# Kernel tuning notes

Measured on AMD Instinct MI355X. Metric: run time of the kernel, lower is better.

## Reference

```python
import jax, jax.numpy as jnp
import numpy as np

RANK = 32
ALPHA = 1.0
SCALE = ALPHA / RANK


def setup_inputs() -> dict:
    key = jax.random.key(0)
    k1, k2, k3, k4, k5 = jax.random.split(key, 5)
    B_, S, D_in, D_out = 4, 2048, 4096, 4096
    x = jax.random.normal(k1, (B_, S, D_in), dtype=jnp.float32)
    # nn.Linear weight: [out, in], kaiming-ish scale
    W = jax.random.normal(k2, (D_out, D_in), dtype=jnp.float32) / np.sqrt(D_in)
    bias = jax.random.normal(k3, (D_out,), dtype=jnp.float32) * 0.01
    A = jax.random.normal(k4, (D_in, RANK), dtype=jnp.float32) * 0.01
    # torch init is zeros for B; use small random so output depends on LoRA path
    Bm = jax.random.normal(k5, (RANK, D_out), dtype=jnp.float32) * 0.01
    return {"x": x, "W": W, "bias": bias, "A": A, "B": Bm}


def reference(x, W, bias, A, B):
    # Original: y = x @ (W + scale*(A@B)^T)^T + bias
    # Mathematically identical fused form (two GEMMs, no [in,out] delta):
    base = jnp.einsum('bsd,od->bso', x, W)          # [B,S,out]
    lora = jnp.einsum('bsr,ro->bso', x @ A, B)       # [B,S,rank]->[B,S,out]
    return base + SCALE * lora + bias
```

## Files before the change

kernel.cpp:

```cpp
#include <hip/hip_runtime.h>
#include <hip/hip_bf16.h>
#include <stdint.h>

#define RANK 32
#define SCALE (1.0f / 32.0f)

#define BM 128
#define BN 128
#define BK 32

typedef __bf16 bf16x8 __attribute__((ext_vector_type(8)));
typedef float f32x4 __attribute__((ext_vector_type(4)));

__device__ __forceinline__ void gload16(const void* g, void* l) {
  __builtin_amdgcn_global_load_lds(
      (const __attribute__((address_space(1))) unsigned int*)g,
      (__attribute__((address_space(3))) unsigned int*)l, 16, 0, 0);
}

__device__ __forceinline__ unsigned short f2bf(float f) {
  __hip_bfloat16 h = __float2bfloat16(f);
  return *reinterpret_cast<unsigned short*>(&h);
}

__global__ __launch_bounds__(256) void transpose_B_k(const float* __restrict__ B,
                                                     float* __restrict__ Bt,
                                                     int Dout) {
  int idx = blockIdx.x * 256 + threadIdx.x;
  int r = idx / Dout;
  int o = idx - r * Dout;
  Bt[(long long)o * RANK + r] = B[idx];
}

__global__ __launch_bounds__(256) void merge_W_k(const float* __restrict__ W,
                                                 const float* __restrict__ A,
                                                 const float* __restrict__ Bt,
                                                 unsigned short* __restrict__ Wb,
                                                 int Din, int Dout) {
  __shared__ float sB[16 * RANK];
  int nib = Din / 256;
  int ib = blockIdx.x % nib;
  int ob = blockIdx.x / nib;
  int i0 = ib * 256, o0 = ob * 16;
  int t = threadIdx.x;

  if (t < 128) {
    reinterpret_cast<float4*>(sB)[t] =
        reinterpret_cast<const float4*>(Bt + (long long)o0 * RANK)[t];
  }

  float a[RANK];
  const float4* Ap = reinterpret_cast<const float4*>(A + (long long)(i0 + t) * RANK);
#pragma unroll
  for (int c = 0; c < RANK / 4; ++c) {
    float4 v = Ap[c];
    a[c * 4 + 0] = v.x; a[c * 4 + 1] = v.y;
    a[c * 4 + 2] = v.z; a[c * 4 + 3] = v.w;
  }
  __syncthreads();

  for (int o = 0; o < 16; ++o) {
    float d = 0.f;
#pragma unroll
    for (int j = 0; j < RANK; ++j) d += a[j] * sB[o * RANK + j];
    long long off = (long long)(o0 + o) * Din + i0 + t;
    Wb[off] = f2bf(W[off] + SCALE * d);
  }
}

__global__ __launch_bounds__(256) void cast_x_k(const float* __restrict__ in,
                                                unsigned short* __restrict__ out,
                                                long long n8) {
  long long i = (long long)blockIdx.x * 256 + threadIdx.x;
  if (i >= n8) return;
  const float4* in4 = reinterpret_cast<const float4*>(in) + i * 2;
  float4 v0 = in4[0], v1 = in4[1];
  union { unsigned short u[8]; uint4 q; } p;
  p.u[0] = f2bf(v0.x); p.u[1] = f2bf(v0.y); p.u[2] = f2bf(v0.z); p.u[3] = f2bf(v0.w);
  p.u[4] = f2bf(v1.x); p.u[5] = f2bf(v1.y); p.u[6] = f2bf(v1.z); p.u[7] = f2bf(v1.w);
  reinterpret_cast<uint4*>(out)[i] = p.q;
}

__global__ __launch_bounds__(256, 2) void gemm_bt_bias_k(
    const unsigned short* __restrict__ Xb,
    const unsigned short* __restrict__ Wb,
    const float* __restrict__ bias,
    float* __restrict__ Out,
    int M, int N, int K) {
  __shared__ unsigned short As[BM * BK];
  __shared__ unsigned short Bs[BN * BK];

  int nbn = N / BN;
  int bm = blockIdx.x / nbn;
  int bn = blockIdx.x % nbn;
  int tid = threadIdx.x;
  int wid = tid >> 6;
  int lane = tid & 63;
  int wr = wid >> 1, wc = wid & 1;

  const unsigned short* ga = Xb + (long long)bm * BM * K;
  const unsigned short* gb = Wb + (long long)bn * BN * K;
  int rlo = lane >> 2;
  int col = (lane & 3) * 8;

  f32x4 acc[4][4] = {};

  for (int kt = 0; kt < K; kt += BK) {
    gload16(ga + (long long)(wid * 16 + rlo) * K + kt + col, &As[wid * 512]);
    gload16(ga + (long long)(64 + wid * 16 + rlo) * K + kt + col, &As[(4 + wid) * 512]);
    gload16(gb + (long long)(wid * 16 + rlo) * K + kt + col, &Bs[wid * 512]);
    gload16(gb + (long long)(64 + wid * 16 + rlo) * K + kt + col, &Bs[(4 + wid) * 512]);
    __syncthreads();

    int arow = wr * 64 + (lane & 15);
    int brow = wc * 64 + (lane & 15);
    int koff = (lane >> 4) * 8;
    bf16x8 af[4], bfr[4];
#pragma unroll
    for (int i = 0; i < 4; ++i)
      af[i] = *reinterpret_cast<const bf16x8*>(&As[(arow + i * 16) * BK + koff]);
#pragma unroll
    for (int j = 0; j < 4; ++j)
      bfr[j] = *reinterpret_cast<const bf16x8*>(&Bs[(brow + j * 16) * BK + koff]);
#pragma unroll
    for (int i = 0; i < 4; ++i)
#pragma unroll
      for (int j = 0; j < 4; ++j)
        acc[i][j] = __builtin_amdgcn_mfma_f32_16x16x32_bf16(af[i], bfr[j], acc[i][j], 0, 0, 0);
    __syncthreads();
  }

  int orow = bm * BM + wr * 64;
  int ocol = bn * BN + wc * 64;
#pragma unroll
  for (int j = 0; j < 4; ++j) {
    int gc = ocol + j * 16 + (lane & 15);
    float bv = bias[gc];
#pragma unroll
    for (int i = 0; i < 4; ++i) {
      int gr = orow + i * 16 + (lane >> 4) * 4;
#pragma unroll
      for (int v = 0; v < 4; ++v)
        Out[(long long)(gr + v) * N + gc] = acc[i][j][v] + bv;
    }
  }
}

extern "C" void kernel_launch(void* const* d_in, const int* in_sizes, int n_in,
                              void* d_out, int out_size, void* d_ws, size_t ws_size,
                              hipStream_t stream) {
  const float* x    = (const float*)d_in[0];
  const float* W    = (const float*)d_in[1];
  const float* bias = (const float*)d_in[2];
  const float* A    = (const float*)d_in[3];
  const float* B    = (const float*)d_in[4];

  int Din  = in_sizes[3] / RANK;
  int Dout = in_sizes[4] / RANK;
  long long M = (long long)in_sizes[0] / Din;

  size_t xb_bytes = (size_t)M * Din * 2;
  size_t wb_bytes = (size_t)Dout * Din * 2;
  size_t bt_bytes = (size_t)Dout * RANK * 4;
  if (ws_size < xb_bytes + wb_bytes + bt_bytes) return;

  char* ws = (char*)d_ws;
  unsigned short* Xb = (unsigned short*)ws;
  unsigned short* Wb = (unsigned short*)(ws + xb_bytes);
  float* Bt          = (float*)(ws + xb_bytes + wb_bytes);

  transpose_B_k<<<dim3((Dout * RANK) / 256), dim3(256), 0, stream>>>(B, Bt, Dout);
  merge_W_k<<<dim3((Dout / 16) * (Din / 256)), dim3(256), 0, stream>>>(W, A, Bt, Wb, Din, Dout);
  long long n8 = M * Din / 8;
  cast_x_k<<<dim3((unsigned)(n8 / 256)), dim3(256), 0, stream>>>(x, Xb, n8);
  gemm_bt_bias_k<<<dim3((unsigned)((M / BM) * (Dout / BN))), dim3(256), 0, stream>>>(
      Xb, Wb, bias, (float*)d_out, (int)M, Dout, Din);
}
```

Before: 382.6 us.

## Replace GEMM with 256x256 double-buffered swizzled-LDS pipelined MFMA kernel

Replaces the 128x128x32 single-buffered bf16 GEMM with a 256x256x64 tile kernel using 8 waves. Global-to-LDS loads are double-buffered and interleaved with four MFMA phases under explicit barriers, waitcnt and setprio. LDS rows are XOR-swizzled to avoid bank conflicts, and block IDs are remapped for L2 locality. The aim is to overlap memory with compute and raise arithmetic intensity. In exchange it uses 128KB of LDS and many accumulator registers, with fragile hand-written synchronisation.

```diff
diff --git a/kernel.cpp b/kernel.cpp
--- a/kernel.cpp
+++ b/kernel.cpp
@@ -4,10 +4,6 @@
 
 #define RANK 32
 #define SCALE (1.0f / 32.0f)
-
-#define BM 128
-#define BN 128
-#define BK 32
 
 typedef __bf16 bf16x8 __attribute__((ext_vector_type(8)));
 typedef float f32x4 __attribute__((ext_vector_type(4)));
@@ -81,67 +77,158 @@
   reinterpret_cast<uint4*>(out)[i] = p.q;
 }
 
-__global__ __launch_bounds__(256, 2) void gemm_bt_bias_k(
+template <int NISSUE>
+__device__ __forceinline__ void stage(const unsigned short* g, int K, int koff,
+                                      int row0, unsigned short* ldsbase,
+                                      int t, int wid) {
+  int r = t >> 3;
+  int cg = (t & 7) ^ (r & 7);
+#pragma unroll
+  for (int i = 0; i < NISSUE; ++i) {
+    gload16(g + (long long)(row0 + i * 64 + r) * K + koff + cg * 8,
+            ldsbase + (row0 + i * 64) * 64 + wid * 512);
+  }
+}
+
+__device__ __forceinline__ int swz_off(int rowl, int k) {
+  return rowl * 64 + ((((k) >> 3) ^ (rowl & 7)) << 3);
+}
+
+__global__ __launch_bounds__(512, 2) void gemm256_bias_k(
     const unsigned short* __restrict__ Xb,
     const unsigned short* __restrict__ Wb,
     const float* __restrict__ bias,
     float* __restrict__ Out,
     int M, int N, int K) {
-  __shared__ unsigned short As[BM * BK];
-  __shared__ unsigned short Bs[BN * BK];
-
-  int nbn = N / BN;
-  int bm = blockIdx.x / nbn;
-  int bn = blockIdx.x % nbn;
-  int tid = threadIdx.x;
-  int wid = tid >> 6;
-  int lane = tid & 63;
-  int wr = wid >> 1, wc = wid & 1;
-
-  const unsigned short* ga = Xb + (long long)bm * BM * K;
-  const unsigned short* gb = Wb + (long long)bn * BN * K;
-  int rlo = lane >> 2;
-  int col = (lane & 3) * 8;
-
-  f32x4 acc[4][4] = {};
-
-  for (int kt = 0; kt < K; kt += BK) {
-    gload16(ga + (long long)(wid * 16 + rlo) * K + kt + col, &As[wid * 512]);
-    gload16(ga + (long long)(64 + wid * 16 + rlo) * K + kt + col, &As[(4 + wid) * 512]);
-    gload16(gb + (long long)(wid * 16 + rlo) * K + kt + col, &Bs[wid * 512]);
-    gload16(gb + (long long)(64 + wid * 16 + rlo) * K + kt + col, &Bs[(4 + wid) * 512]);
-    __syncthreads();
-
-    int arow = wr * 64 + (lane & 15);
-    int brow = wc * 64 + (lane & 15);
-    int koff = (lane >> 4) * 8;
-    bf16x8 af[4], bfr[4];
-#pragma unroll
-    for (int i = 0; i < 4; ++i)
-      af[i] = *reinterpret_cast<const bf16x8*>(&As[(arow + i * 16) * BK + koff]);
-#pragma unroll
-    for (int j = 0; j < 4; ++j)
-      bfr[j] = *reinterpret_cast<const bf16x8*>(&Bs[(brow + j * 16) * BK + koff]);
-#pragma unroll
-    for (int i = 0; i < 4; ++i)
-#pragma unroll
-      for (int j = 0; j < 4; ++j)
-        acc[i][j] = __builtin_amdgcn_mfma_f32_16x16x32_bf16(af[i], bfr[j], acc[i][j], 0, 0, 0);
-    __syncthreads();
-  }
-
-  int orow = bm * BM + wr * 64;
-  int ocol = bn * BN + wc * 64;
-#pragma unroll
-  for (int j = 0; j < 4; ++j) {
-    int gc = ocol + j * 16 + (lane & 15);
+  __shared__ unsigned short As[2][256 * 64];
+  __shared__ unsigned short Bs[2][256 * 64];
+
+  int nbn = N / 256;
+  int cpx = gridDim.x >> 3;
+  int bid = blockIdx.x;
+  int swz = (bid & 7) * cpx + (bid >> 3);
+  int bm = swz / nbn, bn = swz % nbn;
+
+  int t = threadIdx.x;
+  int wid = t >> 6, lane = t & 63;
+  int wr = wid >> 2, wc = wid & 3;
+  int lr = lane & 15, kq = (lane >> 4) * 8;
+  int aw = wr * 128, bw = wc * 64;
+
+  const unsigned short* ga = Xb + (long long)bm * 256 * K;
+  const unsigned short* gb = Wb + (long long)bn * 256 * K;
+
+  f32x4 acc[8][4] = {};
+  bf16x8 a[4][2], b0[2][2], b1[2][2];
+
+  const int NT = K / 64;
+
+  stage<4>(ga, K, 0, 0, As[0], t, wid);
+  stage<4>(gb, K, 0, 0, Bs[0], t, wid);
+  stage<4>(ga, K, 64, 0, As[1], t, wid);
+  asm volatile("s_waitcnt vmcnt(4)" ::: "memory");
+  __builtin_amdgcn_s_barrier();
+
+  for (int kt = 0; kt < NT; ++kt) {
+    int cur = kt & 1;
+    const unsigned short* Ac = As[cur];
+    const unsigned short* Bc = Bs[cur];
+    unsigned short* An = As[cur];
+    unsigned short* Bn = Bs[cur ^ 1];
+    int konext = (kt + 1) * 64, konext2 = (kt + 2) * 64;
+
+#pragma unroll
+    for (int m = 0; m < 4; ++m)
+#pragma unroll
+      for (int ks = 0; ks < 2; ++ks)
+        a[m][ks] = *(const bf16x8*)&Ac[swz_off(aw + m * 16 + lr, ks * 32 + kq)];
+#pragma unroll
+    for (int n = 0; n < 2; ++n)
+#pragma unroll
+      for (int ks = 0; ks < 2; ++ks)
+        b0[n][ks] = *(const bf16x8*)&Bc[swz_off(bw + n * 16 + lr, ks * 32 + kq)];
+    if (kt + 1 < NT) stage<2>(gb, K, konext, 0, Bn, t, wid);
+    __builtin_amdgcn_s_barrier();
+    asm volatile("s_waitcnt lgkmcnt(0)" ::: "memory");
+    __builtin_amdgcn_s_setprio(1);
+#pragma unroll
+    for (int m = 0; m < 4; ++m)
+#pragma unroll
+      for (int n = 0; n < 2; ++n)
+#pragma unroll
+        for (int ks = 0; ks < 2; ++ks)
+          acc[m][n] = __builtin_amdgcn_mfma_f32_16x16x32_bf16(a[m][ks], b0[n][ks], acc[m][n], 0, 0, 0);
+    __builtin_amdgcn_s_setprio(0);
+    __builtin_amdgcn_s_barrier();
+
+#pragma unroll
+    for (int n = 0; n < 2; ++n)
+#pragma unroll
+      for (int ks = 0; ks < 2; ++ks)
+        b1[n][ks] = *(const bf16x8*)&Bc[swz_off(bw + 32 + n * 16 + lr, ks * 32 + kq)];
+    if (kt + 1 < NT) stage<2>(gb, K, konext, 128, Bn, t, wid);
+    __builtin_amdgcn_s_barrier();
+    asm volatile("s_waitcnt lgkmcnt(0)" ::: "memory");
+    __builtin_amdgcn_s_setprio(1);
+#pragma unroll
+    for (int m = 0; m < 4; ++m)
+#pragma unroll
+      for (int n = 0; n < 2; ++n)
+#pragma unroll
+        for (int ks = 0; ks < 2; ++ks)
+          acc[m][2 + n] = __builtin_amdgcn_mfma_f32_16x16x32_bf16(a[m][ks], b1[n][ks], acc[m][2 + n], 0, 0, 0);
+    __builtin_amdgcn_s_setprio(0);
+    __builtin_amdgcn_s_barrier();
+
+#pragma unroll
+    for (int m = 0; m < 4; ++m)
+#pragma unroll
+      for (int ks = 0; ks < 2; ++ks)
+        a[m][ks] = *(const bf16x8*)&Ac[swz_off(aw + 64 + m * 16 + lr, ks * 32 + kq)];
+    __builtin_amdgcn_s_barrier();
+    asm volatile("s_waitcnt lgkmcnt(0)" ::: "memory");
+    __builtin_amdgcn_s_setprio(1);
+#pragma unroll
+    for (int m = 0; m < 4; ++m)
+#pragma unroll
+      for (int n = 0; n < 2; ++n)
+#pragma unroll
+        for (int ks = 0; ks < 2; ++ks)
+          acc[4 + m][2 + n] = __builtin_amdgcn_mfma_f32_16x16x32_bf16(a[m][ks], b1[n][ks], acc[4 + m][2 + n], 0, 0, 0);
+    __builtin_amdgcn_s_setprio(0);
+    __builtin_amdgcn_s_barrier();
+
+    if (kt + 2 < NT) {
+      stage<4>(ga, K, konext2, 0, An, t, wid);
+      asm volatile("s_waitcnt vmcnt(4)" ::: "memory");
+    } else if (kt + 1 < NT) {
+      asm volatile("s_waitcnt vmcnt(0)" ::: "memory");
+    }
+    __builtin_amdgcn_s_barrier();
+    __builtin_amdgcn_s_setprio(1);
+#pragma unroll
+    for (int m = 0; m < 4; ++m)
+#pragma unroll
+      for (int n = 0; n < 2; ++n)
+#pragma unroll
+        for (int ks = 0; ks < 2; ++ks)
+          acc[4 + m][n] = __builtin_amdgcn_mfma_f32_16x16x32_bf16(a[m][ks], b0[n][ks], acc[4 + m][n], 0, 0, 0);
+    __builtin_amdgcn_s_setprio(0);
+    __builtin_amdgcn_s_barrier();
+  }
+
+  long long orow = (long long)bm * 256 + wr * 128;
+  int ocol = bn * 256 + wc * 64;
+#pragma unroll
+  for (int n = 0; n < 4; ++n) {
+    int gc = ocol + n * 16 + lr;
     float bv = bias[gc];
 #pragma unroll
-    for (int i = 0; i < 4; ++i) {
-      int gr = orow + i * 16 + (lane >> 4) * 4;
+    for (int m = 0; m < 8; ++m) {
+      long long gr = orow + m * 16 + (lane >> 4) * 4;
 #pragma unroll
       for (int v = 0; v < 4; ++v)
-        Out[(long long)(gr + v) * N + gc] = acc[i][j][v] + bv;
+        Out[(gr + v) * N + gc] = acc[m][n][v] + bv;
     }
   }
 }
@@ -173,6 +260,6 @@
   merge_W_k<<<dim3((Dout / 16) * (Din / 256)), dim3(256), 0, stream>>>(W, A, Bt, Wb, Din, Dout);
   long long n8 = M * Din / 8;
   cast_x_k<<<dim3((unsigned)(n8 / 256)), dim3(256), 0, stream>>>(x, Xb, n8);
-  gemm_bt_bias_k<<<dim3((unsigned)((M / BM) * (Dout / BN))), dim3(256), 0, stream>>>(
+  gemm256_bias_k<<<dim3((unsigned)((M / 256) * (Dout / 256))), dim3(512), 0, stream>>>(
       Xb, Wb, bias, (float*)d_out, (int)M, Dout, Din);
 }
```

New measurement: 362.5 us. -5.3%, faster.
